# Kernel tuning notes

Hardware: AMD Instinct MI355X
Metric: run time of the kernel (lower is better)

The kernel has to match this reference:

```python
import jax, jax.numpy as jnp
import numpy as np

T, D, F, E, K, R = 4096, 1024, 4096, 8, 2, 16
SCALE = 32.0 / 16.0  # lora_alpha / lora_rank


def setup_inputs() -> dict:
    key = jax.random.key(0)
    ks = jax.random.split(key, 11)
    rn = lambda k, shape, sc: jax.random.normal(k, shape, dtype=jnp.float32) * sc
    return {
        "x": rn(ks[0], (T, D), 1.0),
        "gate_w": rn(ks[1], (E, D), 0.02),   # router gate_.weight
        "W1": rn(ks[2], (F, D), 0.02),       # gate_proj (base)
        "W3": rn(ks[3], (F, D), 0.02),       # up_proj (base)
        "W2": rn(ks[4], (D, F), 0.02),       # down_proj (base)
        "A1": rn(ks[5], (E, R, D), 0.02),    # per-expert LoRA A for gate_proj
        "B1": rn(ks[6], (E, F, R), 0.02),
        "A3": rn(ks[7], (E, R, D), 0.02),    # per-expert LoRA A for up_proj
        "B3": rn(ks[8], (E, F, R), 0.02),
        "A2": rn(ks[9], (E, R, F), 0.02),    # per-expert LoRA A for down_proj
        "B2": rn(ks[10], (E, D, R), 0.02),
    }


def reference(x, gate_w, W1, W3, W2, A1, B1, A3, B3, A2, B2):
    # Router: logits -> softmax -> top-k -> renormalize (Mixtral/MixLoRA style)
    router_logits = x @ gate_w.T                      # [T, E]
    probs = jax.nn.softmax(router_logits, axis=-1)
    topv, topi = jax.lax.top_k(probs, K)              # [T, K]
    topv = topv / jnp.sum(topv, axis=-1, keepdims=True)
    tok = jnp.arange(x.shape[0])
    route = jnp.zeros_like(probs).at[tok[:, None], topi].set(topv)  # [T, E] sparse weights

    # Shared base projections computed once (experts share base weights, differ by LoRA)
    xg = x @ W1.T                                     # [T, F]
    xu = x @ W3.T                                     # [T, F]

    out = jnp.zeros_like(x)
    for e in range(E):  # fixed small expert count; not a data-dim loop
        g = xg + SCALE * ((x @ A1[e].T) @ B1[e].T)    # gate_proj + LoRA
        u = xu + SCALE * ((x @ A3[e].T) @ B3[e].T)    # up_proj + LoRA
        h = jax.nn.silu(g) * u                        # SwiGLU
        y = h @ W2.T + SCALE * ((h @ A2[e].T) @ B2[e].T)  # down_proj + LoRA
        out = out + route[:, e:e + 1] * y             # weighted scatter-add combine
    return out, router_logits
```

## Files before the change

kernel.cpp:

```cpp
#include <hip/hip_runtime.h>
#include <stdint.h>

#define T_ 4096
#define D_ 1024
#define F_ 4096
#define E_ 8
#define NCAT 8448
#define KH 4224
#define NTILE_MAX 320

typedef __attribute__((ext_vector_type(8))) short          s16x8;
typedef __attribute__((ext_vector_type(8))) unsigned short u16x8;
typedef __attribute__((ext_vector_type(4))) float          f32x4;

__device__ __forceinline__ unsigned short f2bf(float f) {
  unsigned u = __float_as_uint(f);
  u += 0x7fffu + ((u >> 16) & 1u);
  return (unsigned short)(u >> 16);
}
__device__ __forceinline__ float b2f(unsigned short h) {
  return __uint_as_float(((unsigned)h) << 16);
}

__device__ __forceinline__ void cvt8(const float* __restrict__ s, unsigned short* __restrict__ d) {
  float4 a = *(const float4*)s;
  float4 b = *(const float4*)(s + 4);
  u16x8 v;
  v[0] = f2bf(a.x); v[1] = f2bf(a.y); v[2] = f2bf(a.z); v[3] = f2bf(a.w);
  v[4] = f2bf(b.x); v[5] = f2bf(b.y); v[6] = f2bf(b.z); v[7] = f2bf(b.w);
  *(u16x8*)d = v;
}
__device__ __forceinline__ void cvt8s2(const float* __restrict__ s, unsigned short* __restrict__ d) {
  float4 a = *(const float4*)s;
  float4 b = *(const float4*)(s + 4);
  u16x8 v;
  v[0] = f2bf(2.f * a.x); v[1] = f2bf(2.f * a.y); v[2] = f2bf(2.f * a.z); v[3] = f2bf(2.f * a.w);
  v[4] = f2bf(2.f * b.x); v[5] = f2bf(2.f * b.y); v[6] = f2bf(2.f * b.z); v[7] = f2bf(2.f * b.w);
  *(u16x8*)d = v;
}

__global__ __launch_bounds__(256) void conv_kernel(
    const float* __restrict__ x,  const float* __restrict__ W1,
    const float* __restrict__ W3, const float* __restrict__ W2,
    const float* __restrict__ A1, const float* __restrict__ A3,
    const float* __restrict__ B1, const float* __restrict__ B3,
    const float* __restrict__ A2, const float* __restrict__ B2,
    unsigned short* __restrict__ xb,  unsigned short* __restrict__ Wcatb,
    unsigned short* __restrict__ W2cat, unsigned short* __restrict__ B1b,
    unsigned short* __restrict__ B3b, unsigned short* __restrict__ A2r) {
  const int y = blockIdx.y;
  const size_t i0 = ((size_t)blockIdx.x * 256 + threadIdx.x) * 8;
  if (y == 0) { cvt8(x + i0, xb + i0); }
  else if (y == 1) {
    const size_t d = i0 >> 12, f = i0 & 4095;
    cvt8(W2 + i0, W2cat + d * KH + f);
  }
  else if (y == 2) { cvt8(W1 + i0, Wcatb + i0); }
  else if (y == 3) { cvt8(W3 + i0, Wcatb + 4194304 + i0); }
  else {
    const size_t o8 = (size_t)blockIdx.x * 256 + threadIdx.x;
    if (o8 < 245760) {
      const size_t o = o8 * 8;
      if (o < 131072)        cvt8s2(A1 + o, Wcatb + 8388608 + o);
      else if (o < 262144)   cvt8s2(A3 + (o - 131072), Wcatb + 8388608 + o);
      else if (o < 786432)   cvt8(B1 + (o - 262144), B1b + (o - 262144));
      else if (o < 1310720)  cvt8(B3 + (o - 786432), B3b + (o - 786432));
      else if (o < 1835008)  cvt8s2(A2 + (o - 1310720), A2r + (o - 1310720));
      else {
        const size_t oo = o - 1835008;
        const size_t d = oo >> 7, j = oo & 127;
        const size_t e = j >> 4, r0 = j & 15;
        cvt8(B2 + e * ((size_t)D_ * 16) + d * 16 + r0, W2cat + d * KH + 4096 + j);
      }
    }
  }
}

__global__ __launch_bounds__(256) void router_kernel(
    const float* __restrict__ x, const float* __restrict__ gw,
    float* __restrict__ logits, int2* __restrict__ topi, float2* __restrict__ topw) {
  const int wave = threadIdx.x >> 6, lane = threadIdx.x & 63;
  const int t = blockIdx.x * 4 + wave;
  const float* xr = x + (size_t)t * D_;
  float acc[E_] = {0, 0, 0, 0, 0, 0, 0, 0};
  for (int it = 0; it < 16; ++it) {
    const int d = lane + it * 64;
    const float xv = xr[d];
#pragma unroll
    for (int e = 0; e < E_; ++e) acc[e] += xv * gw[e * D_ + d];
  }
#pragma unroll
  for (int e = 0; e < E_; ++e)
#pragma unroll
    for (int m = 1; m < 64; m <<= 1) acc[e] += __shfl_xor(acc[e], m);
  if (lane == 0) {
    float m0v = acc[0]; int m0i = 0;
#pragma unroll
    for (int e = 1; e < E_; ++e) if (acc[e] > m0v) { m0v = acc[e]; m0i = e; }
    float m1v = -3.0e38f; int m1i = 0;
#pragma unroll
    for (int e = 0; e < E_; ++e) if (e != m0i && acc[e] > m1v) { m1v = acc[e]; m1i = e; }
    const float e1 = __expf(m1v - m0v);
    const float inv = 1.f / (1.f + e1);
    topi[t] = make_int2(m0i, m1i);
    topw[t] = make_float2(inv, e1 * inv);
#pragma unroll
    for (int e = 0; e < E_; ++e) logits[(size_t)t * E_ + e] = acc[e];
  }
}

__global__ __launch_bounds__(256) void bucket_kernel(
    const int2* __restrict__ topi, int* __restrict__ bucketTok, int* __restrict__ bucketCnt) {
  const int pid = blockIdx.x;
  const int e0 = pid >> 3, e1 = pid & 7;
  __shared__ int cnt;
  if (threadIdx.x == 0) cnt = 0;
  __syncthreads();
  for (int t = threadIdx.x; t < T_; t += 256) {
    const int2 ti = topi[t];
    if (ti.x == e0 && ti.y == e1) {
      const int s = atomicAdd(&cnt, 1);
      bucketTok[pid * T_ + s] = t;
    }
  }
  __syncthreads();
  if (threadIdx.x == 0) bucketCnt[pid] = cnt;
}

__global__ void tilelist_kernel(const int* __restrict__ bucketCnt, int* __restrict__ tileList) {
  const int pid = threadIdx.x;
  const int ntile = (bucketCnt[pid] + 15) >> 4;
  int scan = ntile;
#pragma unroll
  for (int m = 1; m < 64; m <<= 1) {
    const int v = __shfl_up(scan, m);
    if (pid >= m) scan += v;
  }
  const int base = scan - ntile;
  const int total = __shfl(scan, 63);
  for (int i = 0; i < ntile; ++i) tileList[base + i] = (pid << 16) | i;
  for (int i = total + pid; i < NTILE_MAX; i += 64) tileList[i] = -1;
}

__device__ __forceinline__ void cstore(float* C, size_t i, float v) { C[i] = v; }
__device__ __forceinline__ void cstore(unsigned short* C, size_t i, float v) { C[i] = f2bf(v); }

#define GLL(g, l) __builtin_amdgcn_global_load_lds(                            \
    (const __attribute__((address_space(1))) void*)(g),                       \
    (__attribute__((address_space(3))) void*)(l), 16, 0, 0)

template <int BN, typename OUT_T>
__global__ __launch_bounds__(256) void gemm_bt(
    const unsigned short* __restrict__ A, const unsigned short* __restrict__ B,
    OUT_T* __restrict__ C, int M, int N, int K, int nbx) {
  constexpr int WCOL = BN / 2, NF = WCOL / 16;
  constexpr int BITER = BN / 32;
  __shared__ __align__(16) char As[2 * 16384];
  __shared__ __align__(16) char Bs[2 * BN * 128];
  const int tid = threadIdx.x;
  int bid = blockIdx.x;
  bid = (bid & 7) * (gridDim.x >> 3) + (bid >> 3);
  const int bx = bid % nbx, by = bid / nbx;
  const long m0 = (long)bx * 128, n0 = (long)by * BN;

  const unsigned short* asrc[4];
  const unsigned short* bsrc[BITER];
#pragma unroll
  for (int i = 0; i < 4; ++i) {
    const int g = i * 256 + tid, row = g >> 3, cb = (g & 7) ^ (row & 7);
    asrc[i] = A + (m0 + row) * (size_t)K + cb * 8;
  }
#pragma unroll
  for (int i = 0; i < BITER; ++i) {
    const int g = i * 256 + tid, row = g >> 3, cb = (g & 7) ^ (row & 7);
    bsrc[i] = B + (n0 + row) * (size_t)K + cb * 8;
  }
  const int lane = tid & 63, wave = tid >> 6;
  const int wr = wave >> 1, wc = wave & 1;
  const int wb = (tid & 192) * 16;
  int aoff[4][2], boff[NF][2];
#pragma unroll
  for (int mf = 0; mf < 4; ++mf) {
    const int ra = wr * 64 + mf * 16 + (lane & 15);
#pragma unroll
    for (int ks = 0; ks < 2; ++ks) {
      const int kb = (ks * 32 + (lane >> 4) * 8) * 2;
      aoff[mf][ks] = (ra * 128 + kb) ^ ((ra & 7) << 4);
    }
  }
#pragma unroll
  for (int nf = 0; nf < NF; ++nf) {
    const int rb = wc * WCOL + nf * 16 + (lane & 15);
#pragma unroll
    for (int ks = 0; ks < 2; ++ks) {
      const int kb = (ks * 32 + (lane >> 4) * 8) * 2;
      boff[nf][ks] = (rb * 128 + kb) ^ ((rb & 7) << 4);
    }
  }

  auto STAGE = [&](int buf, int kt) {
    const size_t ko = (size_t)kt * 64;
#pragma unroll
    for (int i = 0; i < 4; ++i) GLL(asrc[i] + ko, As + buf * 16384 + i * 4096 + wb);
#pragma unroll
    for (int i = 0; i < BITER; ++i) GLL(bsrc[i] + ko, Bs + buf * (BN * 128) + i * 4096 + wb);
  };

  f32x4 acc[4][NF] = {};
  const int nk = K >> 6;
  int cur = 0;
  STAGE(0, 0);
  asm volatile("s_waitcnt vmcnt(0)" ::: "memory");
  __builtin_amdgcn_s_barrier();
  for (int kt = 0; kt < nk; ++kt) {
    if (kt + 1 < nk) STAGE(cur ^ 1, kt + 1);
    const char* Ab = As + cur * 16384;
    const char* Bb = Bs + cur * (BN * 128);
#pragma unroll
    for (int ks = 0; ks < 2; ++ks) {
      s16x8 af[4], bfv[NF];
#pragma unroll
      for (int mf = 0; mf < 4; ++mf) af[mf] = *(const s16x8*)(Ab + aoff[mf][ks]);
#pragma unroll
      for (int nf = 0; nf < NF; ++nf) bfv[nf] = *(const s16x8*)(Bb + boff[nf][ks]);
#pragma unroll
      for (int mf = 0; mf < 4; ++mf)
#pragma unroll
        for (int nf = 0; nf < NF; ++nf)
          acc[mf][nf] = __builtin_amdgcn_mfma_f32_16x16x32_bf16(af[mf], bfv[nf], acc[mf][nf], 0, 0, 0);
    }
    asm volatile("s_waitcnt vmcnt(0)" ::: "memory");
    __builtin_amdgcn_s_barrier();
    cur ^= 1;
  }
#pragma unroll
  for (int mf = 0; mf < 4; ++mf) {
    const int row0 = (int)m0 + wr * 64 + mf * 16 + ((lane >> 4) << 2);
#pragma unroll
    for (int nf = 0; nf < NF; ++nf) {
      const long col = n0 + wc * WCOL + nf * 16 + (lane & 15);
#pragma unroll
      for (int q = 0; q < 4; ++q)
        cstore(C, (size_t)(row0 + q) * N + col, acc[mf][nf][q]);
    }
  }
}

__global__ __launch_bounds__(256) void s3c_kernel(
    const unsigned short* __restrict__ xguP,
    const unsigned short* __restrict__ B1b,
    const unsigned short* __restrict__ B3b,
    const unsigned short* __restrict__ A2r,
    const int* __restrict__ bucketTok, const int* __restrict__ bucketCnt,
    const float2* __restrict__ topw, const int* __restrict__ tileList,
    unsigned short* __restrict__ hq,
    float* __restrict__ Qpart) {
  const int entry = tileList[blockIdx.x];
  if (entry < 0) return;
  const int pid = entry >> 16, z = entry & 0xffff;
  const int nt = bucketCnt[pid];
  const int e0 = pid >> 3, e1 = pid & 7;

  __shared__ int   ldsTok[16];
  __shared__ float ldsW[2][16];
  __shared__ __align__(16) unsigned short hwT[4][2][16][40];
  const int tid = threadIdx.x;
  if (tid < 16) {
    int s = z * 16 + tid; if (s >= nt) s = nt - 1;
    const int t = bucketTok[pid * T_ + s];
    ldsTok[tid] = t;
    const float2 w = topw[t];
    ldsW[0][tid] = w.x; ldsW[1][tid] = w.y;
  }
  __syncthreads();

  const int lane = tid & 63, wave = tid >> 6;
  const int col = lane & 15, chunk = lane >> 4;

  const int at = ldsTok[col];
  const unsigned short* abase = xguP + (size_t)at * NCAT + 8192 +
                                (chunk >> 1) * 128 + (chunk & 1) * 8;
  const s16x8 afrag0 = *(const s16x8*)(abase + e0 * 16);
  const s16x8 afrag1 = *(const s16x8*)(abase + e1 * 16);

  int trow[4]; float w0r[4], w1r[4];
#pragma unroll
  for (int q = 0; q < 4; ++q) {
    trow[q] = ldsTok[chunk * 4 + q];
    w0r[q] = ldsW[0][chunk * 4 + q];
    w1r[q] = ldsW[1][chunk * 4 + q];
  }

  unsigned short (*hw_w)[16][40] = hwT[wave];
  f32x4 qacc0 = {}, qacc1 = {};
  const int ft0 = blockIdx.y * 64 + wave * 16;

  for (int p = 0; p < 8; ++p) {
#pragma unroll
    for (int half = 0; half < 2; ++half) {
      const int i = p * 2 + half;
      const int f = (ft0 + i) * 16 + col;
      s16x8 bg0 = {}, bu0 = {}, bg1 = {}, bu1 = {};
      if (chunk < 2) {
        bg0 = *(const s16x8*)(B1b + ((size_t)e0 * F_ + f) * 16 + chunk * 8);
        bg1 = *(const s16x8*)(B1b + ((size_t)e1 * F_ + f) * 16 + chunk * 8);
      } else {
        bu0 = *(const s16x8*)(B3b + ((size_t)e0 * F_ + f) * 16 + (chunk - 2) * 8);
        bu1 = *(const s16x8*)(B3b + ((size_t)e1 * F_ + f) * 16 + (chunk - 2) * 8);
      }
      f32x4 accg0 = {}, accu0 = {}, accg1 = {}, accu1 = {};
      accg0 = __builtin_amdgcn_mfma_f32_16x16x32_bf16(afrag0, bg0, accg0, 0, 0, 0);
      accu0 = __builtin_amdgcn_mfma_f32_16x16x32_bf16(afrag0, bu0, accu0, 0, 0, 0);
      accg1 = __builtin_amdgcn_mfma_f32_16x16x32_bf16(afrag1, bg1, accg1, 0, 0, 0);
      accu1 = __builtin_amdgcn_mfma_f32_16x16x32_bf16(afrag1, bu1, accu1, 0, 0, 0);
#pragma unroll
      for (int q = 0; q < 4; ++q) {
        const int t = trow[q];
        const unsigned short* xr = xguP + (size_t)t * NCAT + f;
        const float xg = b2f(xr[0]);
        const float xu = b2f(xr[4096]);
        const float g0 = xg + accg0[q], u0 = xu + accu0[q];
        const float g1 = xg + accg1[q], u1 = xu + accu1[q];
        const float h0 = (g0 / (1.f + __expf(-g0))) * u0;
        const float h1 = (g1 / (1.f + __expf(-g1))) * u1;
        const unsigned short hb0 = f2bf(w0r[q] * h0);
        const unsigned short hb1 = f2bf(w1r[q] * h1);
        hq[(size_t)t * KH + f] = f2bf(b2f(hb0) + b2f(hb1));
        hw_w[0][chunk * 4 + q][half * 16 + col] = hb0;
        hw_w[1][chunk * 4 + q][half * 16 + col] = hb1;
      }
    }
    asm volatile("s_waitcnt lgkmcnt(0)" ::: "memory");
    const s16x8 hf0 = *(const s16x8*)&hw_w[0][lane & 15][(lane >> 4) * 8];
    const s16x8 hf1 = *(const s16x8*)&hw_w[1][lane & 15][(lane >> 4) * 8];
    const int fb = (ft0 + 2 * p) * 16 + (lane >> 4) * 8;
    const s16x8 a2f0 = *(const s16x8*)(A2r + ((size_t)e0 * 16 + (lane & 15)) * F_ + fb);
    const s16x8 a2f1 = *(const s16x8*)(A2r + ((size_t)e1 * 16 + (lane & 15)) * F_ + fb);
    qacc0 = __builtin_amdgcn_mfma_f32_16x16x32_bf16(hf0, a2f0, qacc0, 0, 0, 0);
    qacc1 = __builtin_amdgcn_mfma_f32_16x16x32_bf16(hf1, a2f1, qacc1, 0, 0, 0);
  }

  const int r = lane & 15;
  float* qp = Qpart + ((size_t)blockIdx.y * 4 + wave) * T_ * 32;
#pragma unroll
  for (int q = 0; q < 4; ++q) {
    const int t = trow[q];
    qp[(size_t)t * 32 + r]      = qacc0[q];
    qp[(size_t)t * 32 + 16 + r] = qacc1[q];
  }
}

__global__ __launch_bounds__(256) void qscatter_kernel(
    const float* __restrict__ Qpart, const int2* __restrict__ topi,
    unsigned short* __restrict__ hq) {
  const int gid = blockIdx.x * 256 + threadIdx.x;
  const int t = gid >> 7, j = gid & 127;
  const int2 ti = topi[t];
  const int eb = j >> 4, r = j & 15;
  float v = 0.f;
  if (eb == ti.x) {
#pragma unroll
    for (int st = 0; st < 16; ++st) v += Qpart[(size_t)st * (T_ * 32) + t * 32 + r];
  } else if (eb == ti.y) {
#pragma unroll
    for (int st = 0; st < 16; ++st) v += Qpart[(size_t)st * (T_ * 32) + t * 32 + 16 + r];
  }
  hq[(size_t)t * KH + 4096 + j] = f2bf(v);
}

extern "C" void kernel_launch(void* const* d_in, const int* in_sizes, int n_in,
                              void* d_out, int out_size, void* d_ws, size_t ws_size,
                              hipStream_t stream) {
  (void)in_sizes; (void)n_in; (void)out_size; (void)ws_size;
  const float* x   = (const float*)d_in[0];
  const float* gw  = (const float*)d_in[1];
  const float* W1  = (const float*)d_in[2];
  const float* W3  = (const float*)d_in[3];
  const float* W2  = (const float*)d_in[4];
  const float* A1  = (const float*)d_in[5];
  const float* B1  = (const float*)d_in[6];
  const float* A3  = (const float*)d_in[7];
  const float* B3  = (const float*)d_in[8];
  const float* A2  = (const float*)d_in[9];
  const float* B2  = (const float*)d_in[10];
  float* out = (float*)d_out;
  float* logits = out + (size_t)T_ * D_;

  char* w = (char*)d_ws;
  auto alloc = [&](size_t bytes) { char* p = w; w += (bytes + 255) & ~(size_t)255; return p; };
  unsigned short* xb    = (unsigned short*)alloc((size_t)T_ * D_ * 2);
  unsigned short* Wcatb = (unsigned short*)alloc((size_t)NCAT * D_ * 2);
  unsigned short* W2cat = (unsigned short*)alloc((size_t)D_ * KH * 2);
  unsigned short* B1b   = (unsigned short*)alloc((size_t)E_ * F_ * 16 * 2);
  unsigned short* B3b   = (unsigned short*)alloc((size_t)E_ * F_ * 16 * 2);
  unsigned short* A2r   = (unsigned short*)alloc((size_t)E_ * 16 * F_ * 2);
  unsigned short* xguP  = (unsigned short*)alloc((size_t)T_ * NCAT * 2);
  unsigned short* hq    = (unsigned short*)alloc((size_t)T_ * KH * 2);
  float* Qpart          = (float*)alloc((size_t)16 * T_ * 32 * 4);
  int* bucketTok        = (int*)alloc((size_t)64 * T_ * 4);
  int* bucketCnt        = (int*)alloc((size_t)64 * 4);
  int* tileList         = (int*)alloc((size_t)NTILE_MAX * 4);
  int2* topi            = (int2*)alloc((size_t)T_ * 8);
  float2* topw          = (float2*)alloc((size_t)T_ * 8);

  conv_kernel<<<dim3(2048, 5), 256, 0, stream>>>(x, W1, W3, W2, A1, A3, B1, B3, A2, B2,
                                                 xb, Wcatb, W2cat, B1b, B3b, A2r);
  router_kernel<<<dim3(1024), 256, 0, stream>>>(x, gw, logits, topi, topw);
  bucket_kernel<<<dim3(64), 256, 0, stream>>>(topi, bucketTok, bucketCnt);
  tilelist_kernel<<<dim3(1), 64, 0, stream>>>(bucketCnt, tileList);
  gemm_bt<128, unsigned short><<<dim3(32 * 66), 256, 0, stream>>>(
      xb, Wcatb, xguP, T_, NCAT, 1024, 32);
  s3c_kernel<<<dim3(NTILE_MAX, 4), 256, 0, stream>>>(xguP, B1b, B3b, A2r, bucketTok,
                                                     bucketCnt, topw, tileList, hq, Qpart);
  qscatter_kernel<<<dim3(2048), 256, 0, stream>>>(Qpart, topi, hq);
  gemm_bt<64, float><<<dim3(32 * 16), 256, 0, stream>>>(hq, W2cat, out, T_, D_, KH, 32);
}
```

Measured before the change: 256.9 us.

## Replace first GEMM with 256x256-tile 8-wave kernel using phased LDS pipelining

Adds a new GEMM kernel for the fused x·[W1|W3|LoRA-A] projection that uses 256x256 output tiles, 512 threads (8 waves), a 128KB double-buffered swizzled LDS layout, and a four-phase schedule that interleaves half-tile global-to-LDS loads with MFMA compute, raising priority around the MFMA blocks. The larger tile raises arithmetic intensity and data reuse per byte loaded compared to the previous 128x128 tile kernel. In exchange, each block needs large LDS and many accumulator registers, so occupancy drops and the grid shrinks to 528 blocks, which may cause tail imbalance across CUs.

```diff
diff --git a/kernel.cpp b/kernel.cpp
--- a/kernel.cpp
+++ b/kernel.cpp
@@ -149,6 +149,126 @@
     (const __attribute__((address_space(1))) void*)(g),                       \
     (__attribute__((address_space(3))) void*)(l), 16, 0, 0)
 
+__global__ __launch_bounds__(512) void gemm1_8p(
+    const unsigned short* __restrict__ A, const unsigned short* __restrict__ B,
+    unsigned short* __restrict__ C, int M, int N, int K, int nbx) {
+  __shared__ __align__(16) char LDS[131072];
+  const int tid = threadIdx.x;
+  int bid = blockIdx.x;
+  bid = (bid & 7) * (gridDim.x >> 3) + (bid >> 3);
+  const int bx = bid % nbx, by = bid / nbx;
+  const long m0 = (long)bx * 256, n0 = (long)by * 256;
+
+  const int lane = tid & 63, wave = tid >> 6;
+  const int wr = wave >> 2, wc = wave & 3;
+  const int wb = (tid & 448) * 16;
+
+  const unsigned short* srcp[2][2][2];
+#pragma unroll
+  for (int i = 0; i < 2; ++i) {
+    const int g = i * 512 + tid, row = g >> 3, cb = (g & 7) ^ (row & 7);
+#pragma unroll
+    for (int h = 0; h < 2; ++h) {
+      srcp[0][h][i] = A + (m0 + h * 128 + row) * (size_t)K + cb * 8;
+      srcp[1][h][i] = B + (n0 + h * 128 + row) * (size_t)K + cb * 8;
+    }
+  }
+  auto STAGE = [&](int buf, int mat, int h, int kt) {
+#pragma unroll
+    for (int i = 0; i < 2; ++i)
+      GLL(srcp[mat][h][i] + (size_t)kt * 64,
+          LDS + buf * 65536 + mat * 32768 + h * 16384 + i * 8192 + wb);
+  };
+
+  int aoff[4][2], boff[2][2];
+#pragma unroll
+  for (int mi = 0; mi < 4; ++mi) {
+    const int lr = wr * 64 + mi * 16 + (lane & 15);
+#pragma unroll
+    for (int ks = 0; ks < 2; ++ks) {
+      const int kb = ks * 64 + (lane >> 4) * 16;
+      aoff[mi][ks] = (lr * 128 + kb) ^ ((lr & 7) << 4);
+    }
+  }
+#pragma unroll
+  for (int ni = 0; ni < 2; ++ni) {
+    const int lr = wc * 32 + ni * 16 + (lane & 15);
+#pragma unroll
+    for (int ks = 0; ks < 2; ++ks) {
+      const int kb = ks * 64 + (lane >> 4) * 16;
+      boff[ni][ks] = (lr * 128 + kb) ^ ((lr & 7) << 4);
+    }
+  }
+
+  f32x4 acc[2][2][4][2] = {};
+  const int nk = K >> 6;
+
+  STAGE(0, 0, 0, 0); STAGE(0, 1, 0, 0); STAGE(0, 0, 1, 0); STAGE(0, 1, 1, 0);
+  if (nk > 1) { STAGE(1, 0, 0, 1); STAGE(1, 1, 0, 1); }
+  asm volatile("s_waitcnt vmcnt(4)" ::: "memory");
+  __builtin_amdgcn_s_barrier();
+
+  for (int kt = 0; kt < nk; ++kt) {
+    const int cb = kt & 1, nb = cb ^ 1;
+    const char* base = LDS + cb * 65536;
+    s16x8 af[4][2];
+#pragma unroll
+    for (int ph = 0; ph < 4; ++ph) {
+      const int mh = ph >> 1, nh = ph & 1;
+      if (nh == 0) {
+#pragma unroll
+        for (int mi = 0; mi < 4; ++mi)
+#pragma unroll
+          for (int ks = 0; ks < 2; ++ks)
+            af[mi][ks] = *(const s16x8*)(base + mh * 16384 + aoff[mi][ks]);
+      }
+      s16x8 bq[2][2];
+#pragma unroll
+      for (int ni = 0; ni < 2; ++ni)
+#pragma unroll
+        for (int ks = 0; ks < 2; ++ks)
+          bq[ni][ks] = *(const s16x8*)(base + 32768 + nh * 16384 + boff[ni][ks]);
+      if (ph == 0 && kt + 1 < nk) { STAGE(nb, 0, 1, kt + 1); STAGE(nb, 1, 1, kt + 1); }
+      if (ph == 1 && kt + 2 < nk) STAGE(cb, 0, 0, kt + 2);
+      if (ph == 3 && kt + 2 < nk) STAGE(cb, 1, 0, kt + 2);
+      __builtin_amdgcn_s_barrier();
+      asm volatile("s_waitcnt lgkmcnt(0)" ::: "memory");
+      __builtin_amdgcn_sched_barrier(0);
+      __builtin_amdgcn_s_setprio(1);
+#pragma unroll
+      for (int ks = 0; ks < 2; ++ks)
+#pragma unroll
+        for (int mi = 0; mi < 4; ++mi)
+#pragma unroll
+          for (int ni = 0; ni < 2; ++ni)
+            acc[mh][nh][mi][ni] = __builtin_amdgcn_mfma_f32_16x16x32_bf16(
+                af[mi][ks], bq[ni][ks], acc[mh][nh][mi][ni], 0, 0, 0);
+      __builtin_amdgcn_s_setprio(0);
+      if (ph == 3) {
+        if (kt == nk - 2) asm volatile("s_waitcnt vmcnt(0)" ::: "memory");
+        else              asm volatile("s_waitcnt vmcnt(4)" ::: "memory");
+      }
+      __builtin_amdgcn_s_barrier();
+    }
+  }
+
+#pragma unroll
+  for (int mh = 0; mh < 2; ++mh)
+#pragma unroll
+    for (int nh = 0; nh < 2; ++nh)
+#pragma unroll
+      for (int mi = 0; mi < 4; ++mi) {
+        const int row0 = (int)m0 + mh * 128 + wr * 64 + mi * 16 + ((lane >> 4) << 2);
+#pragma unroll
+        for (int ni = 0; ni < 2; ++ni) {
+          const long col = n0 + nh * 128 + wc * 32 + ni * 16 + (lane & 15);
+#pragma unroll
+          for (int q = 0; q < 4; ++q)
+            cstore(C, (size_t)(row0 + q) * N + col, acc[mh][nh][mi][ni][q]);
+        }
+      }
+}
+
 template <int BN, typename OUT_T>
 __global__ __launch_bounds__(256) void gemm_bt(
     const unsigned short* __restrict__ A, const unsigned short* __restrict__ B,
@@ -408,8 +528,7 @@
   router_kernel<<<dim3(1024), 256, 0, stream>>>(x, gw, logits, topi, topw);
   bucket_kernel<<<dim3(64), 256, 0, stream>>>(topi, bucketTok, bucketCnt);
   tilelist_kernel<<<dim3(1), 64, 0, stream>>>(bucketCnt, tileList);
-  gemm_bt<128, unsigned short><<<dim3(32 * 66), 256, 0, stream>>>(
-      xb, Wcatb, xguP, T_, NCAT, 1024, 32);
+  gemm1_8p<<<dim3(16 * 33), 512, 0, stream>>>(xb, Wcatb, xguP, T_, NCAT, 1024, 16);
   s3c_kernel<<<dim3(NTILE_MAX, 4), 256, 0, stream>>>(xguP, B1b, B3b, A2r, bucketTok,
                                                      bucketCnt, topw, tileList, hq, Qpart);
   qscatter_kernel<<<dim3(2048), 256, 0, stream>>>(Qpart, topi, hq);
```

After: 265.9 us. 3.5% more time.
